# Optimization experiments

Hardware: AMD Instinct MI355X
Metric: run time of the kernel (lower is better)

Reference implementation:

```python
import jax, jax.numpy as jnp
import numpy as np

B, N1, N2, C, P, H, MLP = 8, 4096, 4096, 512, 256, 8, 2048
HD = C // H  # head dim = 64
EPS = 1e-12


def _l2norm(x):
    # torch F.normalize(dim=-1): x / max(||x||_2, eps)
    n = jnp.sqrt(jnp.sum(x * x, axis=-1, keepdims=True))
    return x / jnp.maximum(n, EPS)


def setup_inputs() -> dict:
    key = jax.random.key(0)
    ks = jax.random.split(key, 8)
    w = lambda i, shape: jax.random.normal(ks[i], shape, jnp.float32) * 0.02
    return {
        "x1": jax.random.normal(ks[0], (B, N1, C), jnp.float32),
        "x2": jax.random.normal(ks[1], (B, N2, C), jnp.float32),
        "Wq": w(2, (C, C)), "bq": jnp.zeros((C,), jnp.float32),
        "Wkv": w(3, (C, 2 * C)), "bkv": jnp.zeros((2 * C,), jnp.float32),
        # proj_k and proj_v share ONE Linear(N_2, proj_size) in the source
        "Wp": w(4, (N2, P)), "bp": jnp.zeros((P,), jnp.float32),
        "pos_q": jnp.zeros((1, N1, C), jnp.float32),
        "pos_k": jnp.zeros((1, N2, C), jnp.float32),
        "temperature": jnp.ones((H, 1, 1), jnp.float32),
        "W1": w(5, (C, MLP)), "b1": jnp.zeros((MLP,), jnp.float32),
        "W2": w(6, (MLP, C)), "b2": jnp.zeros((C,), jnp.float32),
    }


def reference(x1, x2, Wq, bq, Wkv, bkv, Wp, bp, pos_q, pos_k, temperature,
              W1, b1, W2, b2):
    # q += pos_embed_q is in-place in torch, so q_skip includes pos embedding
    q = x1 @ Wq + bq + pos_q                      # [B,N1,C]
    q_skip = q
    kv = x2 @ Wkv + bkv                           # [B,N2,2C]
    k = kv[..., :C] + pos_k                       # [B,N2,C]
    v = kv[..., C:]                               # [B,N2,C]

    qh = q.reshape(B, N1, H, HD).transpose(0, 2, 1, 3)   # [B,H,N1,hd]
    kh = k.reshape(B, N2, H, HD).transpose(0, 2, 1, 3)   # [B,H,N2,hd]
    vh = v.reshape(B, N2, H, HD).transpose(0, 2, 1, 3)   # [B,H,N2,hd]

    # project K^T and V^T along the sequence axis (shared weights)
    kp = jnp.einsum('bhnd,np->bhdp', kh, Wp) + bp        # [B,H,hd,P]
    vp_t = jnp.einsum('bhnd,np->bhdp', vh, Wp) + bp      # [B,H,hd,P]

    attn = jnp.einsum('bhqd,bhdp->bhqp', qh, kp) * temperature  # [B,H,N1,P]
    attn = jax.nn.softmax(attn, axis=-1)                 # dropout: eval mode

    x = jnp.einsum('bhqp,bhdp->bhqd', attn, vp_t)        # [B,H,N1,hd]
    # source does permute(0,3,1,2).reshape(B,N1,C) -- replicate exactly
    x = x.transpose(0, 3, 1, 2).reshape(B, N1, C)

    x = _l2norm(x + q_skip)                              # Add & L2-Norm
    h = jax.nn.gelu(x @ W1 + b1, approximate=False)      # nn.GELU (exact)
    out = _l2norm(h @ W2 + b2 + x)                       # FFN -> Add & L2-Norm
    return out
```

## Files before the change

kernel.cpp:

```cpp
#include <hip/hip_runtime.h>
#include <hip/hip_bf16.h>
#include <math.h>

#define B_    8
#define N1_   4096
#define N2_   4096
#define C_    512
#define P_    256
#define H_    8
#define MLP_  2048
#define HD_   64

typedef __hip_bfloat16 bf16;
typedef __attribute__((ext_vector_type(8))) short short8;
typedef __attribute__((ext_vector_type(4))) float f32x4;

__device__ __forceinline__ float bf2f(bf16 v) { return __bfloat162float(v); }
__device__ __forceinline__ bf16  f2bf(float v) { return __float2bfloat16(v); }
__device__ __forceinline__ float ubf2f(unsigned short u) {
  union { float f; unsigned int i; } cv; cv.i = ((unsigned int)u) << 16; return cv.f;
}
__device__ __forceinline__ unsigned short f2bfu(float v) {
  union { bf16 b; unsigned short u; } cv; cv.b = __float2bfloat16(v); return cv.u;
}
__device__ __forceinline__ float gelu_fast(float x) {
  const float u = fabsf(x) * 0.70710678118654752f;
  const float t = __builtin_amdgcn_rcpf(__builtin_fmaf(0.3275911f, u, 1.0f));
  float p = __builtin_fmaf(1.061405429f, t, -1.453152027f);
  p = __builtin_fmaf(p, t, 1.421413741f);
  p = __builtin_fmaf(p, t, -0.284496736f);
  p = __builtin_fmaf(p, t, 0.254829592f);
  p *= t;
  const float e = __expf(-u * u);
  float erfv = __builtin_fmaf(-p, e, 1.0f);
  erfv = (x < 0.0f) ? -erfv : erfv;
  return 0.5f * x * (1.0f + erfv);
}

__device__ __forceinline__ void gload16(const void* g, void* l) {
  __builtin_amdgcn_global_load_lds(
      (const __attribute__((address_space(1))) void*)g,
      (__attribute__((address_space(3))) void*)l, 16, 0, 0);
}

__global__ __launch_bounds__(256) void f2b_kernel(
    const float* __restrict__ in, bf16* __restrict__ out, int n4)
{
  int i = blockIdx.x * 256 + threadIdx.x;
  const int stride = gridDim.x * 256;
  for (; i < n4; i += stride) {
    const float4 v = ((const float4*)in)[i];
    ushort4 o;
    o.x = f2bfu(v.x); o.y = f2bfu(v.y); o.z = f2bfu(v.z); o.w = f2bfu(v.w);
    ((ushort4*)out)[i] = o;
  }
}

__global__ __launch_bounds__(256) void transpose_f2b_kernel(
    const float* __restrict__ in, bf16* __restrict__ out, int K, int N, int ldin)
{
  __shared__ float tile[32][33];
  const int kb = blockIdx.y * 32, nb = blockIdx.x * 32;
  const int tx = threadIdx.x & 31, ty = threadIdx.x >> 5;
  #pragma unroll
  for (int i = 0; i < 4; ++i)
    tile[ty + 8 * i][tx] = in[(size_t)(kb + ty + 8 * i) * ldin + nb + tx];
  __syncthreads();
  #pragma unroll
  for (int i = 0; i < 4; ++i)
    out[(size_t)(nb + ty + 8 * i) * K + kb + tx] = f2bf(tile[tx][ty + 8 * i]);
}

template<int BN, int OUTF32, int ACT, int POS, int TRANSC>
__global__ __launch_bounds__(256) void mfma_gemm_kernel(
    const bf16* __restrict__ A, const bf16* __restrict__ Bt,
    const float* __restrict__ bias, const float* __restrict__ pos, int posmask,
    void* __restrict__ Cv, int M, int N, int K)
{
  constexpr int WGN = BN / 64;
  constexpr int WGR = 4 / WGN;
  constexpr int FM  = 128 / (16 * WGR);
  __shared__ bf16 As[128 * 32];
  __shared__ bf16 Bs[BN * 32];
  const int t  = threadIdx.x;
  const int l  = t & 63;
  const int w  = t >> 6;
  const int wr = w / WGN, wc = w % WGN;
  const int lr = l & 15, kg = l >> 4;

  const int gx  = gridDim.x;
  const int nwg = gx * gridDim.y;
  const int h   = blockIdx.y * gx + blockIdx.x;
  int bx = blockIdx.x, by = blockIdx.y;
  if ((nwg & 7) == 0) {
    const int tid = (h & 7) * (nwg >> 3) + (h >> 3);
    bx = tid % gx; by = tid / gx;
  }
  const int m0 = by * 128, n0 = bx * BN;

  const bf16* ga = A  + (size_t)(m0 + (t >> 2)) * K + (t & 3) * 8;
  const bf16* gb = Bt + (size_t)(n0 + (t >> 2)) * K + (t & 3) * 8;
  char* asl = (char*)As + t * 16;
  char* bsl = (char*)Bs + t * 16;

  f32x4 acc[FM][4] = {};

  for (int k0 = 0; k0 < K; k0 += 32) {
    gload16(ga, asl);
    gload16(ga + (size_t)64 * K, asl + 4096);
    gload16(gb, bsl);
    if (BN == 128) gload16(gb + (size_t)64 * K, bsl + 4096);
    ga += 32; gb += 32;
    __syncthreads();
    short8 af[FM], bfv[4];
    #pragma unroll
    for (int i = 0; i < FM; ++i)
      af[i] = *(const short8*)&As[(wr * (FM * 16) + i * 16 + lr) * 32 + kg * 8];
    #pragma unroll
    for (int j = 0; j < 4; ++j)
      bfv[j] = *(const short8*)&Bs[(wc * 64 + j * 16 + lr) * 32 + kg * 8];
    #pragma unroll
    for (int i = 0; i < FM; ++i)
      #pragma unroll
      for (int j = 0; j < 4; ++j)
        acc[i][j] = __builtin_amdgcn_mfma_f32_16x16x32_bf16(
            af[i], bfv[j], acc[i][j], 0, 0, 0);
    __syncthreads();
  }

  #pragma unroll
  for (int i = 0; i < FM; ++i) {
    #pragma unroll
    for (int j = 0; j < 4; ++j) {
      const int n = n0 + wc * 64 + j * 16 + lr;
      const float bv = bias[n];
      if (TRANSC) {
        const int mb = m0 + wr * (FM * 16) + i * 16 + kg * 4;
        ushort4 pk;
        #pragma unroll
        for (int r = 0; r < 4; ++r) {
          const int m = mb + r;
          float v = acc[i][j][r] + bv;
          if (POS) v += pos[(size_t)(m & posmask) * N + n];
          ((unsigned short*)&pk)[r] = f2bfu(v);
        }
        *(ushort4*)&((bf16*)Cv)[((size_t)(mb >> 12) * N + n) * (size_t)N1_ + (mb & 4095)] = pk;
      } else {
        #pragma unroll
        for (int r = 0; r < 4; ++r) {
          const int m = m0 + wr * (FM * 16) + i * 16 + kg * 4 + r;
          float v = acc[i][j][r] + bv;
          if (POS) v += pos[(size_t)(m & posmask) * N + n];
          if (ACT) v = gelu_fast(v);
          if (OUTF32) ((float*)Cv)[(size_t)m * N + n] = v;
          else        ((bf16*)Cv)[(size_t)m * N + n] = f2bf(v);
        }
      }
    }
  }
}

template<int BIASM>
__global__ __launch_bounds__(256) void proj_kernel(
    const bf16* __restrict__ A, const bf16* __restrict__ Bt,
    const float* __restrict__ bias, bf16* __restrict__ Cb,
    int M, int N, int K, long aBatch, long bBatch, long cBatch)
{
  __shared__ bf16 As[64 * 32];
  __shared__ bf16 Bs[64 * 32];
  const int t = threadIdx.x, l = t & 63, w = t >> 6;
  const int wr = w >> 1, wc = w & 1;
  const int lr = l & 15, kg = l >> 4;
  const int z = blockIdx.z;
  const int m0 = blockIdx.y * 64, n0 = blockIdx.x * 64;
  const bf16* ga = A  + (size_t)z * aBatch + (size_t)(m0 + (t >> 2)) * K + (t & 3) * 8;
  const bf16* gb = Bt + (size_t)z * bBatch + (size_t)(n0 + (t >> 2)) * K + (t & 3) * 8;
  char* asl = (char*)As + t * 16;
  char* bsl = (char*)Bs + t * 16;
  f32x4 acc[2][2] = {};
  for (int k0 = 0; k0 < K; k0 += 32) {
    gload16(ga, asl);
    gload16(gb, bsl);
    ga += 32; gb += 32;
    __syncthreads();
    short8 af[2], bfr[2];
    #pragma unroll
    for (int i = 0; i < 2; ++i)
      af[i] = *(const short8*)&As[(wr * 32 + i * 16 + lr) * 32 + kg * 8];
    #pragma unroll
    for (int j = 0; j < 2; ++j)
      bfr[j] = *(const short8*)&Bs[(wc * 32 + j * 16 + lr) * 32 + kg * 8];
    #pragma unroll
    for (int i = 0; i < 2; ++i)
      #pragma unroll
      for (int j = 0; j < 2; ++j)
        acc[i][j] = __builtin_amdgcn_mfma_f32_16x16x32_bf16(
            af[i], bfr[j], acc[i][j], 0, 0, 0);
    __syncthreads();
  }
  #pragma unroll
  for (int i = 0; i < 2; ++i)
    #pragma unroll
    for (int j = 0; j < 2; ++j) {
      const int n = n0 + wc * 32 + j * 16 + lr;
      #pragma unroll
      for (int r = 0; r < 4; ++r) {
        const int m = m0 + wr * 32 + i * 16 + kg * 4 + r;
        const float v = acc[i][j][r] + (BIASM ? bias[m] : bias[n]);
        Cb[(size_t)z * cBatch + (size_t)m * N + n] = f2bf(v);
      }
    }
}

__global__ __launch_bounds__(256) void attn_mfma_kernel(
    const bf16* __restrict__ qb, const bf16* __restrict__ kpT,
    const bf16* __restrict__ vp, const float* __restrict__ temp,
    bf16* __restrict__ xatT)
{
  __shared__ bf16 qs[64 * 64];
  __shared__ bf16 us[256 * 64];
  __shared__ bf16 vs[64 * 256];
  const int t = threadIdx.x, w = t >> 6, l = t & 63;
  const int lr = l & 15, kg = l >> 4;
  const int b = blockIdx.z, h = blockIdx.y;
  const int q0 = blockIdx.x * 64;
  const int bh = b * H_ + h;
  const float tv = temp[h];

  {
    const int rowb = t >> 3, ch = t & 7;
    #pragma unroll
    for (int p = 0; p < 2; ++p) {
      const int r = rowb + 32 * p;
      const short8 v = *(const short8*)(qb + ((size_t)(b * N1_ + q0 + r)) * C_ + h * HD_ + ch * 8);
      *(short8*)((char*)qs + ((r * 128 + ch * 16) ^ ((r & 7) << 4))) = v;
    }
    const bf16* kpb = kpT + (size_t)bh * (P_ * HD_);
    #pragma unroll
    for (int p = 0; p < 8; ++p) {
      const int r = rowb + 32 * p;
      const short8 v = *(const short8*)(kpb + r * HD_ + ch * 8);
      *(short8*)((char*)us + ((r * 128 + ch * 16) ^ ((r & 7) << 4))) = v;
    }
    const bf16* vpb = vp + (size_t)bh * (HD_ * P_);
    const int rowv = t >> 5, chv = t & 31;
    #pragma unroll
    for (int p = 0; p < 8; ++p) {
      const int r = rowv + 8 * p;
      const short8 v = *(const short8*)(vpb + r * P_ + chv * 8);
      *(short8*)((char*)vs + ((r * 512 + chv * 16) ^ ((r & 7) << 4))) = v;
    }
  }
  __syncthreads();

  short8 aq[2];
  {
    const int row = w * 16 + lr;
    const int sw = (row & 7) << 4;
    aq[0] = *(const short8*)((const char*)qs + ((row * 128 +  0 + kg * 16) ^ sw));
    aq[1] = *(const short8*)((const char*)qs + ((row * 128 + 64 + kg * 16) ^ sw));
  }
  f32x4 s[16] = {};
  #pragma unroll
  for (int j = 0; j < 16; ++j) {
    const int row = j * 16 + lr;
    const int sw = (row & 7) << 4;
    const short8 b0 = *(const short8*)((const char*)us + ((row * 128 +  0 + kg * 16) ^ sw));
    const short8 b1 = *(const short8*)((const char*)us + ((row * 128 + 64 + kg * 16) ^ sw));
    s[j] = __builtin_amdgcn_mfma_f32_16x16x32_bf16(aq[0], b0, s[j], 0, 0, 0);
    s[j] = __builtin_amdgcn_mfma_f32_16x16x32_bf16(aq[1], b1, s[j], 0, 0, 0);
  }

  float inv_[4];
  #pragma unroll
  for (int j = 0; j < 16; ++j)
    #pragma unroll
    for (int r = 0; r < 4; ++r) s[j][r] *= tv;
  #pragma unroll
  for (int r = 0; r < 4; ++r) {
    float m = s[0][r];
    #pragma unroll
    for (int j = 1; j < 16; ++j) m = fmaxf(m, s[j][r]);
    #pragma unroll
    for (int off = 1; off < 16; off <<= 1) m = fmaxf(m, __shfl_xor(m, off));
    float sum = 0.f;
    #pragma unroll
    for (int j = 0; j < 16; ++j) { s[j][r] = __expf(s[j][r] - m); sum += s[j][r]; }
    #pragma unroll
    for (int off = 1; off < 16; off <<= 1) sum += __shfl_xor(sum, off);
    inv_[r] = 1.0f / sum;
  }
  __syncthreads();

  #pragma unroll
  for (int r = 0; r < 4; ++r) {
    const int q = w * 16 + kg * 4 + r;
    const int sw = (q & 7) << 4;
    #pragma unroll
    for (int j = 0; j < 16; ++j) {
      const int p = j * 16 + lr;
      ((unsigned short*)us)[((q * 512 + p * 2) ^ sw) >> 1] = f2bfu(s[j][r] * inv_[r]);
    }
  }
  __syncthreads();

  f32x4 o[4] = {};
  #pragma unroll
  for (int kc = 0; kc < 8; ++kc) {
    const int qrow = w * 16 + lr;
    const short8 pb = *(const short8*)((const char*)us +
        ((qrow * 512 + kc * 64 + kg * 16) ^ ((qrow & 7) << 4)));
    #pragma unroll
    for (int i = 0; i < 4; ++i) {
      const int drow = i * 16 + lr;
      const short8 vb = *(const short8*)((const char*)vs +
          ((drow * 512 + kc * 64 + kg * 16) ^ ((drow & 7) << 4)));
      o[i] = __builtin_amdgcn_mfma_f32_16x16x32_bf16(vb, pb, o[i], 0, 0, 0);
    }
  }
  const int qq = q0 + w * 16 + lr;
  bf16* ob = xatT + (size_t)bh * (HD_ * (size_t)N1_) + qq;
  #pragma unroll
  for (int i = 0; i < 4; ++i)
    #pragma unroll
    for (int r = 0; r < 4; ++r) {
      const int d = i * 16 + kg * 4 + r;
      ob[(size_t)d * N1_] = f2bf(o[i][r]);
    }
}

__global__ __launch_bounds__(256) void norm1_kernel(
    const bf16* __restrict__ xatT, const bf16* __restrict__ qb,
    bf16* __restrict__ xb)
{
  const int row = blockIdx.x;
  const int b = row >> 12, np = row & 4095;
  const int d = np >> 6, h = (np >> 3) & 7, qhi = np & 7;
  const int c = threadIdx.x * 2;
  const size_t tbase = ((size_t)(b * H_ + h) * HD_ + d) * N1_ + qhi * 512 + c;
  const size_t qbase = (size_t)row * C_ + c;
  const ushort2 xa = *(const ushort2*)((const unsigned short*)xatT + tbase);
  const ushort2 qa = *(const ushort2*)((const unsigned short*)qb + qbase);
  float v0 = ubf2f(xa.x) + ubf2f(qa.x);
  float v1 = ubf2f(xa.y) + ubf2f(qa.y);
  float ss = v0 * v0 + v1 * v1;
  #pragma unroll
  for (int off = 32; off > 0; off >>= 1) ss += __shfl_xor(ss, off);
  __shared__ float sw[4];
  if ((threadIdx.x & 63) == 0) sw[threadIdx.x >> 6] = ss;
  __syncthreads();
  const float tot = sw[0] + sw[1] + sw[2] + sw[3];
  const float scale = 1.0f / fmaxf(sqrtf(tot), 1e-12f);
  ushort2 o;
  o.x = f2bfu(v0 * scale);
  o.y = f2bfu(v1 * scale);
  *(ushort2*)((unsigned short*)xb + qbase) = o;
}

__global__ __launch_bounds__(256) void norm2_kernel(
    const float* __restrict__ yb, const bf16* __restrict__ xb,
    float* __restrict__ outp)
{
  const int row = blockIdx.x;
  const int c0 = threadIdx.x, c1 = threadIdx.x + 256;
  float v0 = yb[(size_t)row * C_ + c0] + bf2f(xb[(size_t)row * C_ + c0]);
  float v1 = yb[(size_t)row * C_ + c1] + bf2f(xb[(size_t)row * C_ + c1]);
  float ss = v0 * v0 + v1 * v1;
  #pragma unroll
  for (int off = 32; off > 0; off >>= 1) ss += __shfl_xor(ss, off);
  __shared__ float sw[4];
  if ((threadIdx.x & 63) == 0) sw[threadIdx.x >> 6] = ss;
  __syncthreads();
  const float tot = sw[0] + sw[1] + sw[2] + sw[3];
  const float scale = 1.0f / fmaxf(sqrtf(tot), 1e-12f);
  outp[(size_t)row * C_ + c0] = v0 * scale;
  outp[(size_t)row * C_ + c1] = v1 * scale;
}

extern "C" void kernel_launch(void* const* d_in, const int* in_sizes, int n_in,
                              void* d_out, int out_size, void* d_ws, size_t ws_size,
                              hipStream_t stream)
{
  const float* x1   = (const float*)d_in[0];
  const float* x2   = (const float*)d_in[1];
  const float* Wq   = (const float*)d_in[2];
  const float* bq   = (const float*)d_in[3];
  const float* Wkv  = (const float*)d_in[4];
  const float* bkv  = (const float*)d_in[5];
  const float* Wp   = (const float*)d_in[6];
  const float* bp   = (const float*)d_in[7];
  const float* posq = (const float*)d_in[8];
  const float* posk = (const float*)d_in[9];
  const float* temp = (const float*)d_in[10];
  const float* W1   = (const float*)d_in[11];
  const float* b1   = (const float*)d_in[12];
  const float* W2   = (const float*)d_in[13];
  const float* b2   = (const float*)d_in[14];

  char* ws = (char*)d_ws;
  bf16*  Abuf = (bf16*)(ws);
  bf16*  Bbuf = (bf16*)(ws + 33554432);
  bf16*  Cbuf = (bf16*)(ws + 67108864);
  bf16*  kpT  = (bf16*)(ws + 100663296);
  bf16*  vpb  = (bf16*)(ws + 102760448);
  bf16*  WpT  = (bf16*)(ws + 104857600);
  bf16*  Wqt  = (bf16*)(ws + 106954752);
  bf16*  Wkt  = (bf16*)(ws + 107479040);
  bf16*  Wvt  = (bf16*)(ws + 108003328);
  float* outp = (float*)d_out;

  int CH;
  size_t w1t_off, w2t_off, yb_off;
  if (ws_size >= 239075328UL) {
    CH = 32768; w1t_off = 167772160UL; w2t_off = 169869312UL; yb_off = 171966464UL;
  } else if (ws_size >= 138412032UL) {
    CH = 16384; w1t_off = 100663296UL; w2t_off = 102760448UL; yb_off = 104857600UL;
  } else {
    CH = 8192;  w1t_off = 100663296UL; w2t_off = 102760448UL; yb_off = 106954752UL;
  }
  bf16*  W1t = (bf16*)(ws + w1t_off);
  bf16*  W2t = (bf16*)(ws + w2t_off);
  float* yb  = (float*)(ws + yb_off);

  const dim3 blk(256);
  const int Mrows = B_ * N1_;
  bf16* xatT = Bbuf;
  bf16* xb   = Abuf;
  bf16* hb   = Bbuf;
  bf16* qb   = Cbuf;

  f2b_kernel<<<dim3(2048), blk, 0, stream>>>(x2, Abuf, (B_ * N2_ * C_) / 4);
  transpose_f2b_kernel<<<dim3(16, 16), blk, 0, stream>>>(Wkv,      Wkt, C_, C_, 2 * C_);
  transpose_f2b_kernel<<<dim3(16, 16), blk, 0, stream>>>(Wkv + C_, Wvt, C_, C_, 2 * C_);
  transpose_f2b_kernel<<<dim3(16, 16), blk, 0, stream>>>(Wq,       Wqt, C_, C_, C_);
  transpose_f2b_kernel<<<dim3(8, 128), blk, 0, stream>>>(Wp,       WpT, N2_, P_, P_);

  mfma_gemm_kernel<128,0,0,1,1><<<dim3(C_/128, Mrows/128), blk, 0, stream>>>(
      Abuf, Wkt, bkv, posk, N2_ - 1, Cbuf, Mrows, C_, C_);
  proj_kernel<1><<<dim3(1, 4, B_*H_), blk, 0, stream>>>(
      WpT, Cbuf, bp, kpT, P_, HD_, N2_, 0L, (long)HD_*N2_, (long)P_*HD_);
  mfma_gemm_kernel<128,0,0,0,1><<<dim3(C_/128, Mrows/128), blk, 0, stream>>>(
      Abuf, Wvt, bkv + C_, nullptr, 0, Cbuf, Mrows, C_, C_);
  proj_kernel<0><<<dim3(4, 1, B_*H_), blk, 0, stream>>>(
      Cbuf, WpT, bp, vpb, HD_, P_, N2_, (long)HD_*N2_, 0L, (long)HD_*P_);
  f2b_kernel<<<dim3(2048), blk, 0, stream>>>(x1, Abuf, (B_ * N1_ * C_) / 4);
  mfma_gemm_kernel<128,0,0,1,0><<<dim3(C_/128, Mrows/128), blk, 0, stream>>>(
      Abuf, Wqt, bq, posq, N1_ - 1, qb, Mrows, C_, C_);
  attn_mfma_kernel<<<dim3(N1_/64, H_, B_), blk, 0, stream>>>(
      qb, kpT, vpb, temp, xatT);
  transpose_f2b_kernel<<<dim3(64, 16), blk, 0, stream>>>(W1, W1t, C_,   MLP_, MLP_);
  transpose_f2b_kernel<<<dim3(16, 64), blk, 0, stream>>>(W2, W2t, MLP_, C_,   C_);
  norm1_kernel<<<dim3(Mrows), blk, 0, stream>>>(xatT, qb, xb);
  for (int c = 0; c < Mrows / CH; ++c) {
    const bf16* xc = xb + (size_t)c * CH * C_;
    mfma_gemm_kernel<128,0,1,0,0><<<dim3(MLP_/128, CH/128), blk, 0, stream>>>(
        xc, W1t, b1, nullptr, 0, hb, CH, MLP_, C_);
    mfma_gemm_kernel<128,1,0,0,0><<<dim3(C_/128, CH/128), blk, 0, stream>>>(
        hb, W2t, b2, nullptr, 0, yb, CH, C_, MLP_);
    norm2_kernel<<<dim3(CH), blk, 0, stream>>>(
        yb, xc, outp + (size_t)c * CH * C_);
  }
}
```

Measured before the change: 773.4 us.

## Fuse K/V GEMMs, merge projections, fuse FFN2 with L2-norm, use exact GELU

Runs the K and V input projections as a single GEMM over the concatenated Wkv weight, writing into two transposed output buffers. Merges the two sequence-axis projection kernels into one launch. Replaces the separate fp32 FFN2 GEMM and norm2 kernel with a fused kernel that computes a 64x512 output tile per block, adds the residual, and applies L2 normalization in registers, which avoids the fp32 intermediate round trip. It also swaps the polynomial GELU approximation for erff, which is more accurate but may cost more ALU time. The fused kernel keeps a large accumulator (32 f32x4 per thread) and runs far fewer blocks, which risks register pressure and lower occupancy.

```diff
diff --git a/kernel.cpp b/kernel.cpp
--- a/kernel.cpp
+++ b/kernel.cpp
@@ -23,18 +23,8 @@
 __device__ __forceinline__ unsigned short f2bfu(float v) {
   union { bf16 b; unsigned short u; } cv; cv.b = __float2bfloat16(v); return cv.u;
 }
-__device__ __forceinline__ float gelu_fast(float x) {
-  const float u = fabsf(x) * 0.70710678118654752f;
-  const float t = __builtin_amdgcn_rcpf(__builtin_fmaf(0.3275911f, u, 1.0f));
-  float p = __builtin_fmaf(1.061405429f, t, -1.453152027f);
-  p = __builtin_fmaf(p, t, 1.421413741f);
-  p = __builtin_fmaf(p, t, -0.284496736f);
-  p = __builtin_fmaf(p, t, 0.254829592f);
-  p *= t;
-  const float e = __expf(-u * u);
-  float erfv = __builtin_fmaf(-p, e, 1.0f);
-  erfv = (x < 0.0f) ? -erfv : erfv;
-  return 0.5f * x * (1.0f + erfv);
+__device__ __forceinline__ float gelu_exact(float x) {
+  return 0.5f * x * (1.0f + erff(x * 0.70710678118654752f));
 }
 
 __device__ __forceinline__ void gload16(const void* g, void* l) {
@@ -75,7 +65,7 @@
 __global__ __launch_bounds__(256) void mfma_gemm_kernel(
     const bf16* __restrict__ A, const bf16* __restrict__ Bt,
     const float* __restrict__ bias, const float* __restrict__ pos, int posmask,
-    void* __restrict__ Cv, int M, int N, int K)
+    void* __restrict__ Cv, void* __restrict__ Cv2, int M, int N, int K)
 {
   constexpr int WGN = BN / 64;
   constexpr int WGR = 4 / WGN;
@@ -139,19 +129,20 @@
         ushort4 pk;
         #pragma unroll
         for (int r = 0; r < 4; ++r) {
-          const int m = mb + r;
           float v = acc[i][j][r] + bv;
-          if (POS) v += pos[(size_t)(m & posmask) * N + n];
+          if (POS && n < C_) v += pos[(size_t)((mb + r) & posmask) * C_ + n];
           ((unsigned short*)&pk)[r] = f2bfu(v);
         }
-        *(ushort4*)&((bf16*)Cv)[((size_t)(mb >> 12) * N + n) * (size_t)N1_ + (mb & 4095)] = pk;
+        bf16* ob = (bf16*)(n < C_ ? Cv : Cv2);
+        const int nc = n & (C_ - 1);
+        *(ushort4*)&ob[((size_t)(mb >> 12) * C_ + nc) * (size_t)N1_ + (mb & 4095)] = pk;
       } else {
         #pragma unroll
         for (int r = 0; r < 4; ++r) {
           const int m = m0 + wr * (FM * 16) + i * 16 + kg * 4 + r;
           float v = acc[i][j][r] + bv;
           if (POS) v += pos[(size_t)(m & posmask) * N + n];
-          if (ACT) v = gelu_fast(v);
+          if (ACT) v = gelu_exact(v);
           if (OUTF32) ((float*)Cv)[(size_t)m * N + n] = v;
           else        ((bf16*)Cv)[(size_t)m * N + n] = f2bf(v);
         }
@@ -160,21 +151,29 @@
   }
 }
 
-template<int BIASM>
-__global__ __launch_bounds__(256) void proj_kernel(
-    const bf16* __restrict__ A, const bf16* __restrict__ Bt,
-    const float* __restrict__ bias, bf16* __restrict__ Cb,
-    int M, int N, int K, long aBatch, long bBatch, long cBatch)
+__global__ __launch_bounds__(256) void proj_both_kernel(
+    const bf16* __restrict__ WpT, const bf16* __restrict__ kT,
+    const bf16* __restrict__ vT, const float* __restrict__ bp,
+    bf16* __restrict__ kpT, bf16* __restrict__ vpb)
 {
   __shared__ bf16 As[64 * 32];
   __shared__ bf16 Bs[64 * 32];
   const int t = threadIdx.x, l = t & 63, w = t >> 6;
   const int wr = w >> 1, wc = w & 1;
   const int lr = l & 15, kg = l >> 4;
-  const int z = blockIdx.z;
-  const int m0 = blockIdx.y * 64, n0 = blockIdx.x * 64;
-  const bf16* ga = A  + (size_t)z * aBatch + (size_t)(m0 + (t >> 2)) * K + (t & 3) * 8;
-  const bf16* gb = Bt + (size_t)z * bBatch + (size_t)(n0 + (t >> 2)) * K + (t & 3) * 8;
+  const int zz = blockIdx.z;
+  const int isk = (zz < 64) ? 1 : 0;
+  const int z  = isk ? zz : zz - 64;
+  const int K  = N2_;
+  const int m0 = isk ? blockIdx.x * 64 : 0;
+  const int n0 = isk ? 0 : blockIdx.x * 64;
+  const int N  = isk ? HD_ : P_;
+  const bf16* Ab  = isk ? WpT : (vT + (size_t)z * HD_ * N2_);
+  const bf16* Btb = isk ? (kT + (size_t)z * HD_ * N2_) : WpT;
+  bf16* Cb = isk ? (kpT + (size_t)z * P_ * HD_) : (vpb + (size_t)z * HD_ * P_);
+
+  const bf16* ga = Ab  + (size_t)(m0 + (t >> 2)) * K + (t & 3) * 8;
+  const bf16* gb = Btb + (size_t)(n0 + (t >> 2)) * K + (t & 3) * 8;
   char* asl = (char*)As + t * 16;
   char* bsl = (char*)Bs + t * 16;
   f32x4 acc[2][2] = {};
@@ -206,8 +205,8 @@
       #pragma unroll
       for (int r = 0; r < 4; ++r) {
         const int m = m0 + wr * 32 + i * 16 + kg * 4 + r;
-        const float v = acc[i][j][r] + (BIASM ? bias[m] : bias[n]);
-        Cb[(size_t)z * cBatch + (size_t)m * N + n] = f2bf(v);
+        const float v = acc[i][j][r] + (isk ? bp[m] : bp[n]);
+        Cb[(size_t)m * N + n] = f2bf(v);
       }
     }
 }
@@ -357,24 +356,105 @@
   *(ushort2*)((unsigned short*)xb + qbase) = o;
 }
 
-__global__ __launch_bounds__(256) void norm2_kernel(
-    const float* __restrict__ yb, const bf16* __restrict__ xb,
+__global__ __launch_bounds__(256) void mlp2norm_kernel(
+    const bf16* __restrict__ A,
+    const bf16* __restrict__ Bt,
+    const float* __restrict__ bias,
+    const bf16* __restrict__ xr,
     float* __restrict__ outp)
 {
-  const int row = blockIdx.x;
-  const int c0 = threadIdx.x, c1 = threadIdx.x + 256;
-  float v0 = yb[(size_t)row * C_ + c0] + bf2f(xb[(size_t)row * C_ + c0]);
-  float v1 = yb[(size_t)row * C_ + c1] + bf2f(xb[(size_t)row * C_ + c1]);
-  float ss = v0 * v0 + v1 * v1;
-  #pragma unroll
-  for (int off = 32; off > 0; off >>= 1) ss += __shfl_xor(ss, off);
-  __shared__ float sw[4];
-  if ((threadIdx.x & 63) == 0) sw[threadIdx.x >> 6] = ss;
+  __shared__ bf16 As[64 * 32];
+  __shared__ bf16 Bs[512 * 32];
+  __shared__ float rsum[64][2];
+  const int t = threadIdx.x, l = t & 63, w = t >> 6;
+  const int wr = w >> 1, wc = w & 1;
+  const int lr = l & 15, kg = l >> 4;
+  const int K = MLP_;
+
+  int by = blockIdx.x;
+  const int nwg = gridDim.x;
+  if ((nwg & 7) == 0) by = (by & 7) * (nwg >> 3) + (by >> 3);
+  const int m0 = by * 64;
+
+  const bf16* ga = A  + (size_t)(m0 + (t >> 2)) * K + (t & 3) * 8;
+  const bf16* gb = Bt + (size_t)(t >> 2) * K + (t & 3) * 8;
+  char* asl = (char*)As + t * 16;
+  char* bsl = (char*)Bs + t * 16;
+
+  f32x4 acc[2][16] = {};
+
+  for (int k0 = 0; k0 < K; k0 += 32) {
+    gload16(ga, asl);
+    #pragma unroll
+    for (int p = 0; p < 8; ++p)
+      gload16(gb + (size_t)(p * 64) * K, bsl + p * 4096);
+    ga += 32; gb += 32;
+    __syncthreads();
+    short8 af[2];
+    #pragma unroll
+    for (int i = 0; i < 2; ++i)
+      af[i] = *(const short8*)&As[(wr * 32 + i * 16 + lr) * 32 + kg * 8];
+    #pragma unroll
+    for (int j = 0; j < 16; ++j) {
+      const short8 bv = *(const short8*)&Bs[(wc * 256 + j * 16 + lr) * 32 + kg * 8];
+      acc[0][j] = __builtin_amdgcn_mfma_f32_16x16x32_bf16(af[0], bv, acc[0][j], 0, 0, 0);
+      acc[1][j] = __builtin_amdgcn_mfma_f32_16x16x32_bf16(af[1], bv, acc[1][j], 0, 0, 0);
+    }
+    __syncthreads();
+  }
+
+  float psum[2][4] = {};
+  #pragma unroll
+  for (int i = 0; i < 2; ++i)
+    #pragma unroll
+    for (int j = 0; j < 16; ++j) {
+      const int n = wc * 256 + j * 16 + lr;
+      const float bv = bias[n];
+      #pragma unroll
+      for (int r = 0; r < 4; ++r) {
+        const int m = m0 + wr * 32 + i * 16 + kg * 4 + r;
+        const float v = acc[i][j][r] + bv + bf2f(xr[(size_t)m * C_ + n]);
+        acc[i][j][r] = v;
+        psum[i][r] = __builtin_fmaf(v, v, psum[i][r]);
+      }
+    }
+  #pragma unroll
+  for (int i = 0; i < 2; ++i)
+    #pragma unroll
+    for (int r = 0; r < 4; ++r) {
+      float s = psum[i][r];
+      #pragma unroll
+      for (int off = 1; off < 16; off <<= 1) s += __shfl_xor(s, off);
+      psum[i][r] = s;
+    }
+  if (lr == 0) {
+    #pragma unroll
+    for (int i = 0; i < 2; ++i)
+      #pragma unroll
+      for (int r = 0; r < 4; ++r)
+        rsum[wr * 32 + i * 16 + kg * 4 + r][wc] = psum[i][r];
+  }
   __syncthreads();
-  const float tot = sw[0] + sw[1] + sw[2] + sw[3];
-  const float scale = 1.0f / fmaxf(sqrtf(tot), 1e-12f);
-  outp[(size_t)row * C_ + c0] = v0 * scale;
-  outp[(size_t)row * C_ + c1] = v1 * scale;
+  float scl[2][4];
+  #pragma unroll
+  for (int i = 0; i < 2; ++i)
+    #pragma unroll
+    for (int r = 0; r < 4; ++r) {
+      const int row = wr * 32 + i * 16 + kg * 4 + r;
+      const float tot = rsum[row][0] + rsum[row][1];
+      scl[i][r] = 1.0f / fmaxf(sqrtf(tot), 1e-12f);
+    }
+  #pragma unroll
+  for (int i = 0; i < 2; ++i)
+    #pragma unroll
+    for (int j = 0; j < 16; ++j) {
+      const int n = wc * 256 + j * 16 + lr;
+      #pragma unroll
+      for (int r = 0; r < 4; ++r) {
+        const int m = m0 + wr * 32 + i * 16 + kg * 4 + r;
+        outp[(size_t)m * C_ + n] = acc[i][j][r] * scl[i][r];
+      }
+    }
 }
 
 extern "C" void kernel_launch(void* const* d_in, const int* in_sizes, int n_in,
@@ -405,22 +485,18 @@
   bf16*  vpb  = (bf16*)(ws + 102760448);
   bf16*  WpT  = (bf16*)(ws + 104857600);
   bf16*  Wqt  = (bf16*)(ws + 106954752);
-  bf16*  Wkt  = (bf16*)(ws + 107479040);
-  bf16*  Wvt  = (bf16*)(ws + 108003328);
+  bf16*  Wkvt = (bf16*)(ws + 107479040);
   float* outp = (float*)d_out;
 
   int CH;
-  size_t w1t_off, w2t_off, yb_off;
-  if (ws_size >= 239075328UL) {
-    CH = 32768; w1t_off = 167772160UL; w2t_off = 169869312UL; yb_off = 171966464UL;
-  } else if (ws_size >= 138412032UL) {
-    CH = 16384; w1t_off = 100663296UL; w2t_off = 102760448UL; yb_off = 104857600UL;
+  size_t w1t_off, w2t_off;
+  if (ws_size >= 171966464UL) {
+    CH = 32768; w1t_off = 167772160UL; w2t_off = 169869312UL;
   } else {
-    CH = 8192;  w1t_off = 100663296UL; w2t_off = 102760448UL; yb_off = 106954752UL;
+    CH = 8192;  w1t_off = 100663296UL; w2t_off = 102760448UL;
   }
   bf16*  W1t = (bf16*)(ws + w1t_off);
   bf16*  W2t = (bf16*)(ws + w2t_off);
-  float* yb  = (float*)(ws + yb_off);
 
   const dim3 blk(256);
   const int Mrows = B_ * N1_;
@@ -428,24 +504,21 @@
   bf16* xb   = Abuf;
   bf16* hb   = Bbuf;
   bf16* qb   = Cbuf;
+  bf16* kT   = Cbuf;
+  bf16* vT   = Bbuf;
 
   f2b_kernel<<<dim3(2048), blk, 0, stream>>>(x2, Abuf, (B_ * N2_ * C_) / 4);
-  transpose_f2b_kernel<<<dim3(16, 16), blk, 0, stream>>>(Wkv,      Wkt, C_, C_, 2 * C_);
-  transpose_f2b_kernel<<<dim3(16, 16), blk, 0, stream>>>(Wkv + C_, Wvt, C_, C_, 2 * C_);
-  transpose_f2b_kernel<<<dim3(16, 16), blk, 0, stream>>>(Wq,       Wqt, C_, C_, C_);
-  transpose_f2b_kernel<<<dim3(8, 128), blk, 0, stream>>>(Wp,       WpT, N2_, P_, P_);
-
-  mfma_gemm_kernel<128,0,0,1,1><<<dim3(C_/128, Mrows/128), blk, 0, stream>>>(
-      Abuf, Wkt, bkv, posk, N2_ - 1, Cbuf, Mrows, C_, C_);
-  proj_kernel<1><<<dim3(1, 4, B_*H_), blk, 0, stream>>>(
-      WpT, Cbuf, bp, kpT, P_, HD_, N2_, 0L, (long)HD_*N2_, (long)P_*HD_);
-  mfma_gemm_kernel<128,0,0,0,1><<<dim3(C_/128, Mrows/128), blk, 0, stream>>>(
-      Abuf, Wvt, bkv + C_, nullptr, 0, Cbuf, Mrows, C_, C_);
-  proj_kernel<0><<<dim3(4, 1, B_*H_), blk, 0, stream>>>(
-      Cbuf, WpT, bp, vpb, HD_, P_, N2_, (long)HD_*N2_, 0L, (long)HD_*P_);
+  transpose_f2b_kernel<<<dim3(32, 16), blk, 0, stream>>>(Wkv, Wkvt, C_, 2 * C_, 2 * C_);
+  transpose_f2b_kernel<<<dim3(16, 16), blk, 0, stream>>>(Wq,  Wqt,  C_, C_,     C_);
+  transpose_f2b_kernel<<<dim3(8, 128), blk, 0, stream>>>(Wp,  WpT,  N2_, P_,    P_);
+
+  mfma_gemm_kernel<128,0,0,1,1><<<dim3((2*C_)/128, Mrows/128), blk, 0, stream>>>(
+      Abuf, Wkvt, bkv, posk, N2_ - 1, kT, vT, Mrows, 2 * C_, C_);
+  proj_both_kernel<<<dim3(4, 1, 2 * B_ * H_), blk, 0, stream>>>(
+      WpT, kT, vT, bp, kpT, vpb);
   f2b_kernel<<<dim3(2048), blk, 0, stream>>>(x1, Abuf, (B_ * N1_ * C_) / 4);
   mfma_gemm_kernel<128,0,0,1,0><<<dim3(C_/128, Mrows/128), blk, 0, stream>>>(
-      Abuf, Wqt, bq, posq, N1_ - 1, qb, Mrows, C_, C_);
+      Abuf, Wqt, bq, posq, N1_ - 1, qb, nullptr, Mrows, C_, C_);
   attn_mfma_kernel<<<dim3(N1_/64, H_, B_), blk, 0, stream>>>(
       qb, kpT, vpb, temp, xatT);
   transpose_f2b_kernel<<<dim3(64, 16), blk, 0, stream>>>(W1, W1t, C_,   MLP_, MLP_);
@@ -454,10 +527,8 @@
   for (int c = 0; c < Mrows / CH; ++c) {
     const bf16* xc = xb + (size_t)c * CH * C_;
     mfma_gemm_kernel<128,0,1,0,0><<<dim3(MLP_/128, CH/128), blk, 0, stream>>>(
-        xc, W1t, b1, nullptr, 0, hb, CH, MLP_, C_);
-    mfma_gemm_kernel<128,1,0,0,0><<<dim3(C_/128, CH/128), blk, 0, stream>>>(
-        hb, W2t, b2, nullptr, 0, yb, CH, C_, MLP_);
-    norm2_kernel<<<dim3(CH), blk, 0, stream>>>(
-        yb, xc, outp + (size_t)c * CH * C_);
-  }
-}
+        xc, W1t, b1, nullptr, 0, hb, nullptr, CH, MLP_, C_);
+    mlp2norm_kernel<<<dim3(CH/64), blk, 0, stream>>>(
+        hb, W2t, b2, xc, outp + (size_t)c * CH * C_);
+  }
+}
```

Result: slower. 792.2 us (+2.4%).
